# Kernel tuning notes

Hardware: AMD Instinct MI355X
Metric: run time of the kernel (lower is better)

## Reference

```python
import jax, jax.numpy as jnp
import numpy as np

M1 = M2 = M3 = 12   # Fourier modes kept per dim
WID = 32            # channel width
NL = 4              # number of Fourier layers
HID = 128           # skip-block hidden
INF = 9             # coord_dim + param_dim


def _gelu(x):
    return jax.nn.gelu(x, approximate=False)  # torch F.gelu default is exact erf


def _spectral_conv3d(x, w1, w2, w3, w4):
    # x: [B, Cin, S, V, T]; weights: [Cin, Cout, M1, M2, M3, 2]
    B, Ci, S, Vd, T = x.shape
    x_ft = jnp.fft.rfftn(x, axes=(-3, -2, -1))  # [B,Ci,S,V,T//2+1] complex64

    def cmul(sub, w):
        wc = w[..., 0] + 1j * w[..., 1]
        return jnp.einsum('bixyz,ioxyz->boxyz', sub, wc)

    Co = w1.shape[1]
    out_ft = jnp.zeros((B, Co, S, Vd, T // 2 + 1), dtype=x_ft.dtype)
    out_ft = out_ft.at[:, :, :M1, :M2, :M3].set(cmul(x_ft[:, :, :M1, :M2, :M3], w1))
    out_ft = out_ft.at[:, :, -M1:, :M2, :M3].set(cmul(x_ft[:, :, -M1:, :M2, :M3], w2))
    out_ft = out_ft.at[:, :, :M1, -M2:, :M3].set(cmul(x_ft[:, :, :M1, -M2:, :M3], w3))
    out_ft = out_ft.at[:, :, -M1:, -M2:, :M3].set(cmul(x_ft[:, :, -M1:, -M2:, :M3], w4))
    return jnp.fft.irfftn(out_ft, s=(S, Vd, T), axes=(-3, -2, -1))


def setup_inputs() -> dict:
    key = jax.random.key(0)
    ks = jax.random.split(key, 24)
    B, S, Vd, T = 4, 64, 64, 64
    scale = 1.0 / (WID * WID)
    spec_shape = (NL, WID, WID, M1, M2, M3, 2)
    inp = {
        'coords': jax.random.uniform(ks[0], (B, S, Vd, T, 3), dtype=jnp.float32),
        'params': jax.random.normal(ks[1], (B, 6), dtype=jnp.float32),
        'lift_w': 0.3 * jax.random.normal(ks[2], (INF, WID), dtype=jnp.float32),
        'lift_b': jnp.zeros((WID,), jnp.float32),
        'spec_w1': scale * jax.random.uniform(ks[3], spec_shape, dtype=jnp.float32),
        'spec_w2': scale * jax.random.uniform(ks[4], spec_shape, dtype=jnp.float32),
        'spec_w3': scale * jax.random.uniform(ks[5], spec_shape, dtype=jnp.float32),
        'spec_w4': scale * jax.random.uniform(ks[6], spec_shape, dtype=jnp.float32),
        'conv_w': 0.15 * jax.random.normal(ks[7], (NL, WID, WID), dtype=jnp.float32),
        'conv_b': jnp.zeros((NL, WID), jnp.float32),
        's1w': 0.3 * jax.random.normal(ks[8], (NL, INF, HID), dtype=jnp.float32),
        's1b': jnp.zeros((NL, HID), jnp.float32),
        's2w': 0.09 * jax.random.normal(ks[9], (NL, HID, HID), dtype=jnp.float32),
        's2b': jnp.zeros((NL, HID), jnp.float32),
        's3w': 0.09 * jax.random.normal(ks[10], (NL, HID, WID), dtype=jnp.float32),
        's3b': jnp.zeros((NL, WID), jnp.float32),
        'p1w': 0.15 * jax.random.normal(ks[11], (WID, WID // 2), dtype=jnp.float32),
        'p1b': jnp.zeros((WID // 2,), jnp.float32),
        'p2w': 0.25 * jax.random.normal(ks[12], (WID // 2, 1), dtype=jnp.float32),
        'p2b': jnp.zeros((1,), jnp.float32),
    }
    return inp


def reference(coords, params, lift_w, lift_b, spec_w1, spec_w2, spec_w3, spec_w4,
              conv_w, conv_b, s1w, s1b, s2w, s2b, s3w, s3b, p1w, p1b, p2w, p2b):
    B, S, Vd, T, _ = coords.shape
    # coordinate lift: broadcast params over grid, concat -> [B,S,V,T,9]
    pexp = jnp.broadcast_to(params[:, None, None, None, :], (B, S, Vd, T, params.shape[-1]))
    z = jnp.concatenate([coords, pexp], axis=-1)
    x = z @ lift_w + lift_b                      # [B,S,V,T,W]
    x = jnp.transpose(x, (0, 4, 1, 2, 3))        # [B,W,S,V,T]
    for i in range(NL):
        x1 = _spectral_conv3d(x, spec_w1[i], spec_w2[i], spec_w3[i], spec_w4[i])
        x2 = jnp.einsum('bixyz,oi->boxyz', x, conv_w[i]) + conv_b[i][None, :, None, None, None]
        xf = _gelu(x1 + x2)
        skip = _gelu(z @ s1w[i] + s1b[i])
        skip = _gelu(skip @ s2w[i] + s2b[i])
        skip = skip @ s3w[i] + s3b[i]            # [B,S,V,T,W]
        x = xf + jnp.transpose(skip, (0, 4, 1, 2, 3))
    x = jnp.transpose(x, (0, 2, 3, 4, 1))        # [B,S,V,T,W]
    h = _gelu(x @ p1w + p1b)
    out = (h @ p2w + p2b)[..., 0]                # [B,S,V,T]
    return out
```

## Files before the change

### kernel.cpp

```cpp
#include <hip/hip_runtime.h>
#include <hip/hip_bf16.h>
#include <math.h>

#define NB   4
#define NC   32
#define SVT  262144
#define VT   4096
#define NLAY 4
#define TWOPI_64 0.09817477042468103f

typedef __attribute__((ext_vector_type(8))) short bf16x8;
typedef __attribute__((ext_vector_type(4))) float f32x4;
typedef __attribute__((ext_vector_type(4))) unsigned short us4;

__device__ __forceinline__ float gelu_f(float x){
    float x2 = x * x;
    float u  = x * __builtin_fmaf(-0.10294322f, x2, -2.30220795f);
    float e  = __builtin_amdgcn_exp2f(u);
    return x * __builtin_amdgcn_rcpf(1.0f + e);
}

__device__ __forceinline__ unsigned short f2bf(float f){
    union { __hip_bfloat16 h; unsigned short u; } cv;
    cv.h = __float2bfloat16(f);
    return cv.u;
}
__device__ __forceinline__ float bf2f(unsigned short u){
    return __uint_as_float(((unsigned int)u) << 16);
}

__global__ __launch_bounds__(256) void k_prep(
    const float* __restrict__ params,
    const float* __restrict__ s1w, const float* __restrict__ s1b,
    const float* __restrict__ s2w, const float* __restrict__ s3w,
    unsigned short* __restrict__ w2bf,
    unsigned short* __restrict__ w3bf,
    unsigned short* __restrict__ tdft,
    unsigned short* __restrict__ T1h, unsigned short* __restrict__ T1l,
    unsigned short* __restrict__ T2h, unsigned short* __restrict__ T2l,
    float* __restrict__ pbq,
    unsigned short* __restrict__ w1dup)
{
    int g = blockIdx.x * 256 + threadIdx.x;
    if (g < 65536){
        int l = g >> 14, r = g & 16383;
        int c = r >> 7, k = r & 127;
        w2bf[g] = f2bf(s2w[l*16384 + k*128 + c]);
        return;
    }
    g -= 65536;
    if (g < 16384){
        int l = g >> 12, r = g & 4095;
        int c2 = r >> 7, k = r & 127;
        w3bf[g] = f2bf(s3w[l*4096 + k*32 + c2]);
        return;
    }
    g -= 16384;
    if (g < 2048){
        int o = g >> 6, t = g & 63;
        float val = 0.f;
        if (o < 24){
            int kz = o >> 1;
            float ang = (float)((kz * t) & 63) * TWOPI_64;
            float sn, cs; sincosf(ang, &sn, &cs);
            val = (o & 1) ? -sn : cs;
        }
        unsigned short h = f2bf(val);
        tdft[g]        = h;
        tdft[2048 + g] = f2bf(val - bf2f(h));
        return;
    }
    g -= 2048;
    if (g < 8192){
        int col = g >> 6, k1 = g & 63;
        int v = col >> 1, pout = col & 1;
        float val = 0.f;
        if (k1 < 48){
            int ky = k1 >> 1, pin = k1 & 1;
            int kya = (ky < 12) ? ky : ky + 40;
            float ang = (float)((kya * v) & 63) * TWOPI_64;
            float sn, cs; sincosf(ang, &sn, &cs);
            val = pout == 0 ? (pin == 0 ? cs : -sn) : (pin == 0 ? sn : cs);
        }
        unsigned short h = f2bf(val);
        T1h[g] = h;
        T1l[g] = f2bf(val - bf2f(h));
        return;
    }
    g -= 8192;
    if (g < 2048){
        int t = g >> 5, k2 = g & 31;
        float val = 0.f;
        if (k2 < 24){
            int kz = k2 >> 1, part = k2 & 1;
            float wk = (kz == 0) ? 1.f : 2.f;
            float ang = (float)((kz * t) & 63) * TWOPI_64;
            float sn, cs; sincosf(ang, &sn, &cs);
            val = (part ? -sn : cs) * wk * (1.f / 262144.f);
        }
        unsigned short h = f2bf(val);
        T2h[g] = h;
        T2l[g] = f2bf(val - bf2f(h));
        return;
    }
    g -= 2048;
    if (g < 2048){
        int l = g >> 9, b = (g >> 7) & 3, h = g & 127;
        float acc = s1b[l*128 + h];
        #pragma unroll
        for (int j = 0; j < 6; ++j)
            acc += params[b*6 + j] * bf2f(f2bf(s1w[l*1152 + (3 + j)*128 + h]));
        pbq[g] = acc;
        return;
    }
    g -= 2048;
    if (g < 4096){
        int l = g >> 10, rem = g & 1023;
        int h = rem >> 3, slot = rem & 7;
        float val = 0.f;
        if (slot != 3 && slot != 7){
            int row = (slot < 3) ? slot : slot - 4;
            val = bf2f(f2bf(s1w[l*1152 + row*128 + h]));
        }
        w1dup[g] = f2bf(val);
    }
}

__global__ __launch_bounds__(256) void k_lift(
    const float* __restrict__ coords, const float* __restrict__ params,
    const float* __restrict__ lw, const float* __restrict__ lb,
    float* __restrict__ x)
{
    size_t g = (size_t)blockIdx.x * 256 + threadIdx.x;
    int b = (int)(g >> 18);
    size_t p = g & (size_t)(SVT - 1);
    float z[9];
    z[0] = coords[g*3+0]; z[1] = coords[g*3+1]; z[2] = coords[g*3+2];
    #pragma unroll
    for (int j = 0; j < 6; ++j) z[3+j] = params[b*6+j];
    #pragma unroll
    for (int c = 0; c < 32; ++c){
        float acc = lb[c];
        #pragma unroll
        for (int j = 0; j < 9; ++j) acc += z[j] * lw[j*32 + c];
        x[(size_t)(b*32 + c) * SVT + p] = acc;
    }
}

__global__ __launch_bounds__(256) void k_fwdTV(
    const float* __restrict__ x, const unsigned short* __restrict__ tdft,
    float2* __restrict__ X2)
{
    __shared__ __align__(16) unsigned short Ahi[64][72], Alo[64][72];
    __shared__ __align__(16) unsigned short Bhi[32][72], Blo[32][72];
    __shared__ float2 a2[12][66];
    __shared__ float2 wtab[64];
    int tid = threadIdx.x;
    int bc = blockIdx.x >> 6;
    int s  = blockIdx.x & 63;
    if (tid < 64){
        float sn, cs;
        sincosf((float)tid * TWOPI_64, &sn, &cs);
        wtab[tid] = make_float2(cs, sn);
    }
    for (int i = tid; i < 2048; i += 256){
        int o = i >> 6, t = i & 63;
        Bhi[o][t] = tdft[i];
        Blo[o][t] = tdft[2048 + i];
    }
    {
        int row = tid >> 2, c0 = (tid & 3) << 4;
        const float* src = x + (size_t)bc * SVT + (size_t)s * VT + row*64 + c0;
        #pragma unroll
        for (int q = 0; q < 4; ++q){
            float4 v4 = *(const float4*)&src[q*4];
            float vv[4] = {v4.x, v4.y, v4.z, v4.w};
            #pragma unroll
            for (int e = 0; e < 4; ++e){
                unsigned short h = f2bf(vv[e]);
                Ahi[row][c0 + q*4 + e] = h;
                Alo[row][c0 + q*4 + e] = f2bf(vv[e] - bf2f(h));
            }
        }
    }
    __syncthreads();
    int l = tid & 63, w = tid >> 6;
    int lr = l & 15, kg = l >> 4;
    int r0 = w << 4;
    f32x4 acc[2];
    acc[0] = (f32x4){0.f,0.f,0.f,0.f}; acc[1] = (f32x4){0.f,0.f,0.f,0.f};
    #pragma unroll
    for (int kc = 0; kc < 2; ++kc){
        int ko = kc*32 + kg*8;
        bf16x8 ah = *(const bf16x8*)&Ahi[r0 + lr][ko];
        bf16x8 al = *(const bf16x8*)&Alo[r0 + lr][ko];
        #pragma unroll
        for (int n = 0; n < 2; ++n){
            bf16x8 bh = *(const bf16x8*)&Bhi[n*16 + lr][ko];
            bf16x8 bl = *(const bf16x8*)&Blo[n*16 + lr][ko];
            acc[n] = __builtin_amdgcn_mfma_f32_16x16x32_bf16(ah, bh, acc[n], 0, 0, 0);
            acc[n] = __builtin_amdgcn_mfma_f32_16x16x32_bf16(ah, bl, acc[n], 0, 0, 0);
            acc[n] = __builtin_amdgcn_mfma_f32_16x16x32_bf16(al, bh, acc[n], 0, 0, 0);
        }
    }
    #pragma unroll
    for (int n = 0; n < 2; ++n){
        int o = n*16 + lr;
        if (o < 24){
            int kz = o >> 1;
            #pragma unroll
            for (int r = 0; r < 4; ++r){
                int v = r0 + kg*4 + r;
                if (o & 1) a2[kz][v].y = acc[n][r];
                else       a2[kz][v].x = acc[n][r];
            }
        }
    }
    __syncthreads();
    for (int task = tid; task < 288; task += 256){
        int kz = task % 12;
        int ky = task / 12;
        int kya = (ky < 12) ? ky : ky + 40;
        float re = 0.f, im = 0.f;
        for (int v = 0; v < 64; ++v){
            float2 wv = wtab[(kya * v) & 63];
            float2 a  = a2[kz][v];
            re += a.x * wv.x + a.y * wv.y;
            im += a.y * wv.x - a.x * wv.y;
        }
        X2[((size_t)(bc*12 + kz) * 24 + ky) * 64 + s] = make_float2(re, im);
    }
}

__global__ __launch_bounds__(256) void k_fwdS(
    const float2* __restrict__ X2, float2* __restrict__ X3)
{
    __shared__ float2 cin[32][65];
    __shared__ float2 wtab[64];
    int tid = threadIdx.x;
    if (tid < 64){
        float sn, cs; sincosf((float)tid * TWOPI_64, &sn, &cs);
        wtab[tid] = make_float2(cs, sn);
    }
    int rbase = blockIdx.x * 32;
    for (int i = tid; i < 2048; i += 256){
        int row = i >> 6, s = i & 63;
        cin[row][s] = X2[(size_t)(rbase + row) * 64 + s];
    }
    __syncthreads();
    int row = tid & 31;
    int r = rbase + row;
    int kxg = tid >> 5;
    int kxs[3];
    #pragma unroll
    for (int j = 0; j < 3; ++j){ int kxi = kxg*3 + j; kxs[j] = (kxi < 12) ? kxi : kxi + 40; }
    float re[3] = {0,0,0}, im[3] = {0,0,0};
    for (int s = 0; s < 64; ++s){
        float2 cv = cin[row][s];
        #pragma unroll
        for (int j = 0; j < 3; ++j){
            float2 wv = wtab[(kxs[j] * s) & 63];
            re[j] += cv.x * wv.x + cv.y * wv.y;
            im[j] += cv.y * wv.x - cv.x * wv.y;
        }
    }
    int bc = r / 288; int kz = (r / 24) % 12; int ky = r % 24;
    #pragma unroll
    for (int j = 0; j < 3; ++j){
        int kxi = kxg*3 + j;
        X3[(size_t)bc * 6912 + (size_t)kxi * 288 + ky * 12 + kz] = make_float2(re[j], im[j]);
    }
}

__global__ __launch_bounds__(256) void k_modemix(
    const float2* __restrict__ X3,
    const float* __restrict__ w1, const float* __restrict__ w2,
    const float* __restrict__ w3, const float* __restrict__ w4,
    int layer, float2* __restrict__ Y)
{
    __shared__ float2 wlds[32][64];
    int tid = threadIdx.x;
    int m   = tid & 63;
    int b   = tid >> 6;
    int corner = blockIdx.y >> 3;
    int o0     = (blockIdx.y & 7) * 4;
    int moff0  = blockIdx.x * 64;
    const float* wsrc = (corner==0 ? w1 : corner==1 ? w2 : corner==2 ? w3 : w4)
                        + (size_t)layer * 3538944;
    int moff = moff0 + m;
    int m1  = moff / 144;
    int rem = moff - m1 * 144;
    int kx  = m1 + ((corner == 1 || corner == 3) ? 12 : 0);
    int mode_g = kx * 288 + rem + ((corner >= 2) ? 144 : 0);

    float xr[32], xi[32];
    const float2* xp = X3 + (size_t)b * 32 * 6912 + mode_g;
    #pragma unroll
    for (int i = 0; i < 32; ++i){
        float2 a = xp[(size_t)i * 6912];
        xr[i] = a.x; xi[i] = a.y;
    }
    for (int oo = 0; oo < 4; ++oo){
        int o = o0 + oo;
        __syncthreads();
        for (int j = tid; j < 2048; j += 256){
            int i = j >> 6, mm = j & 63;
            wlds[i][mm] = *(const float2*)&wsrc[((size_t)(i*32 + o) * 1728 + moff0 + mm) * 2];
        }
        __syncthreads();
        float re = 0.f, im = 0.f;
        #pragma unroll
        for (int i = 0; i < 32; ++i){
            float2 wv = wlds[i][m];
            re += xr[i]*wv.x - xi[i]*wv.y;
            im += xr[i]*wv.y + xi[i]*wv.x;
        }
        Y[(size_t)(b*32 + o) * 6912 + mode_g] = make_float2(re, im);
    }
}

__global__ __launch_bounds__(256) void k_invS(
    const float2* __restrict__ Y, float2* __restrict__ Z1)
{
    __shared__ float2 yin[24][24];
    __shared__ float2 wtab[64];
    int tid = threadIdx.x;
    if (tid < 64){
        float sn, cs; sincosf((float)tid * TWOPI_64, &sn, &cs);
        wtab[tid] = make_float2(cs, sn);
    }
    int bo = blockIdx.x / 12;
    int kz = blockIdx.x % 12;
    for (int i = tid; i < 576; i += 256){
        int kx = i / 24, ky = i % 24;
        yin[kx][ky] = Y[(size_t)bo * 6912 + (size_t)kx * 288 + ky * 12 + kz];
    }
    __syncthreads();
    int s = tid & 63;
    int kyg = tid >> 6;
    float re[6] = {0,0,0,0,0,0}, im[6] = {0,0,0,0,0,0};
    for (int kxi = 0; kxi < 24; ++kxi){
        int kxa = (kxi < 12) ? kxi : kxi + 40;
        float2 wv = wtab[(kxa * s) & 63];
        #pragma unroll
        for (int j = 0; j < 6; ++j){
            float2 a = yin[kxi][kyg*6 + j];
            re[j] += a.x * wv.x - a.y * wv.y;
            im[j] += a.x * wv.y + a.y * wv.x;
        }
    }
    #pragma unroll
    for (int j = 0; j < 6; ++j){
        int ky = kyg*6 + j;
        Z1[((size_t)(bo*12 + kz) * 64 + s) * 24 + ky] = make_float2(re[j], im[j]);
    }
}

__global__ __launch_bounds__(256) void k_conv(
    float* x, const float* __restrict__ cw,
    const float* __restrict__ cb, int layer)
{
    __shared__ float wsh[32][32];
    __shared__ float bsh[32];
    int tid = threadIdx.x;
    if (tid < 32) bsh[tid] = cb[layer*32 + tid];
    for (int i = tid; i < 1024; i += 256) wsh[i >> 5][i & 31] = cw[layer*1024 + i];
    __syncthreads();
    size_t g = (size_t)blockIdx.x * 256 + tid;
    int b = (int)(g >> 18);
    size_t p = g & (size_t)(SVT - 1);
    float acc[32];
    #pragma unroll
    for (int o = 0; o < 32; ++o) acc[o] = bsh[o];
    for (int i = 0; i < 32; ++i){
        float xv = x[(size_t)(b*32 + i) * SVT + p];
        #pragma unroll
        for (int o = 0; o < 32; ++o) acc[o] += xv * wsh[o][i];
    }
    #pragma unroll
    for (int o = 0; o < 32; ++o) x[(size_t)(b*32 + o) * SVT + p] = acc[o];
}

__global__ __launch_bounds__(256) void k_invVT(
    const float2* __restrict__ Z1,
    const unsigned short* __restrict__ T1h, const unsigned short* __restrict__ T1l,
    const unsigned short* __restrict__ T2h, const unsigned short* __restrict__ T2l,
    float* xio)
{
    __shared__ __align__(16) unsigned short A1h[16][72], A1l[16][72];
    __shared__ __align__(16) unsigned short A2h[64][40], A2l[64][40];
    int tid = threadIdx.x;
    int bo = blockIdx.x >> 6;
    int s  = blockIdx.x & 63;
    for (int i = tid; i < 384; i += 256){
        int r = i / 24, c = 48 + (i % 24);
        A1h[r][c] = 0; A1l[r][c] = 0;
    }
    for (int i = tid; i < 192; i += 256){
        int r = 12 + i / 48, c = i % 48;
        A1h[r][c] = 0; A1l[r][c] = 0;
    }
    for (int i = tid; i < 288; i += 256){
        int kz = i / 24, ky = i % 24;
        float2 a = Z1[((size_t)(bo*12 + kz) * 64 + s) * 24 + ky];
        unsigned short hx = f2bf(a.x), hy = f2bf(a.y);
        A1h[kz][2*ky  ] = hx; A1l[kz][2*ky  ] = f2bf(a.x - bf2f(hx));
        A1h[kz][2*ky+1] = hy; A1l[kz][2*ky+1] = f2bf(a.y - bf2f(hy));
    }
    __syncthreads();
    int l = tid & 63, w = tid >> 6;
    int lr = l & 15, kg = l >> 4;
    f32x4 acc1[2];
    acc1[0] = (f32x4){0.f,0.f,0.f,0.f}; acc1[1] = (f32x4){0.f,0.f,0.f,0.f};
    #pragma unroll
    for (int kc = 0; kc < 2; ++kc){
        int ko = kc*32 + kg*8;
        bf16x8 ah = *(const bf16x8*)&A1h[lr][ko];
        bf16x8 al = *(const bf16x8*)&A1l[lr][ko];
        #pragma unroll
        for (int n = 0; n < 2; ++n){
            int col = (2*w + n)*16 + lr;
            bf16x8 bh = *(const bf16x8*)&T1h[col*64 + ko];
            bf16x8 bl = *(const bf16x8*)&T1l[col*64 + ko];
            acc1[n] = __builtin_amdgcn_mfma_f32_16x16x32_bf16(ah, bh, acc1[n], 0, 0, 0);
            acc1[n] = __builtin_amdgcn_mfma_f32_16x16x32_bf16(ah, bl, acc1[n], 0, 0, 0);
            acc1[n] = __builtin_amdgcn_mfma_f32_16x16x32_bf16(al, bh, acc1[n], 0, 0, 0);
        }
    }
    #pragma unroll
    for (int n = 0; n < 2; ++n){
        int col = (2*w + n)*16 + lr;
        int v = col >> 1, part = col & 1;
        #pragma unroll
        for (int r = 0; r < 4; ++r){
            int k2 = 2*(kg*4 + r) + part;
            float val = acc1[n][r];
            unsigned short h = f2bf(val);
            A2h[v][k2] = h;
            A2l[v][k2] = f2bf(val - bf2f(h));
        }
    }
    int r0 = w << 4;
    bf16x8 ah2 = *(const bf16x8*)&A2h[r0 + lr][kg*8];
    bf16x8 al2 = *(const bf16x8*)&A2l[r0 + lr][kg*8];
    size_t base = (size_t)bo * SVT + (size_t)s * VT;
    #pragma unroll
    for (int n = 0; n < 4; ++n){
        f32x4 a2c = (f32x4){0.f,0.f,0.f,0.f};
        int colt = n*16 + lr;
        bf16x8 bh = *(const bf16x8*)&T2h[colt*32 + kg*8];
        bf16x8 bl = *(const bf16x8*)&T2l[colt*32 + kg*8];
        a2c = __builtin_amdgcn_mfma_f32_16x16x32_bf16(ah2, bh, a2c, 0, 0, 0);
        a2c = __builtin_amdgcn_mfma_f32_16x16x32_bf16(ah2, bl, a2c, 0, 0, 0);
        a2c = __builtin_amdgcn_mfma_f32_16x16x32_bf16(al2, bh, a2c, 0, 0, 0);
        #pragma unroll
        for (int r = 0; r < 4; ++r){
            int v = r0 + kg*4 + r;
            size_t idx = base + (size_t)v*64 + colt;
            xio[idx] = gelu_f(a2c[r] + xio[idx]);
        }
    }
}

template<int LAST>
__global__ __launch_bounds__(256, 8) void k_skip(
    const float* __restrict__ coords,
    const unsigned short* __restrict__ w1dup, const float* __restrict__ pbq,
    const unsigned short* __restrict__ w2bf, const float* __restrict__ s2b,
    const unsigned short* __restrict__ w3bf, const float* __restrict__ s3b,
    int layer, float* __restrict__ xio,
    const float* __restrict__ p1w, const float* __restrict__ p1b,
    const float* __restrict__ p2w, const float* __restrict__ p2b,
    float* __restrict__ out)
{
    __shared__ __align__(16) unsigned short A1[64][136];
    __shared__ __align__(16) unsigned short zst[4][16][8];

    int tid = threadIdx.x;
    size_t g0 = (size_t)blockIdx.x * 64;
    int b = (int)(g0 >> 18);
    const unsigned short* w2g = w2bf + (size_t)layer * 16384;
    const unsigned short* w3g = w3bf + (size_t)layer * 4096;
    const unsigned short* w1g = w1dup + (size_t)layer * 1024;
    const float* pbg = pbq + layer*512 + b*128;
    const float* b2g = s2b + layer*128;

    int l  = tid & 63;
    int w  = tid >> 6;
    int lr = l & 15;
    int kg = l >> 4;

    if (l < 16){
        size_t g = g0 + (size_t)w*16 + l;
        float z0 = coords[g*3+0], z1 = coords[g*3+1], z2 = coords[g*3+2];
        unsigned short h0 = f2bf(z0), h1 = f2bf(z1), h2 = f2bf(z2);
        bf16x8 pk;
        pk[0] = (short)h0; pk[1] = (short)h1; pk[2] = (short)h2; pk[3] = 0;
        pk[4] = (short)f2bf(z0 - bf2f(h0));
        pk[5] = (short)f2bf(z1 - bf2f(h1));
        pk[6] = (short)f2bf(z2 - bf2f(h2));
        pk[7] = 0;
        *(bf16x8*)&zst[w][l][0] = pk;
    }
    bf16x8 bz;
    if (kg == 0) bz = *(const bf16x8*)&zst[w][lr][0];
    else         bz = (bf16x8){0,0,0,0,0,0,0,0};

    {
        f32x4 accB[8];
        #pragma unroll
        for (int m = 0; m < 8; ++m) accB[m] = (f32x4){0.f,0.f,0.f,0.f};
        #pragma unroll
        for (int m = 0; m < 8; ++m){
            bf16x8 af = *(const bf16x8*)&w1g[(m*16 + lr)*8];
            accB[m] = __builtin_amdgcn_mfma_f32_16x16x32_bf16(af, bz, accB[m], 0, 0, 0);
        }
        #pragma unroll
        for (int m = 0; m < 8; ++m){
            int c0 = m*16 + kg*4;
            float4 bb = *(const float4*)&pbg[c0];
            us4 pk4;
            pk4[0] = f2bf(gelu_f(accB[m][0] + bb.x));
            pk4[1] = f2bf(gelu_f(accB[m][1] + bb.y));
            pk4[2] = f2bf(gelu_f(accB[m][2] + bb.z));
            pk4[3] = f2bf(gelu_f(accB[m][3] + bb.w));
            *(us4*)&A1[w*16 + lr][c0] = pk4;
        }
    }
    __syncthreads();

    f32x4 accC[2][4];
    #pragma unroll
    for (int mi = 0; mi < 2; ++mi)
        #pragma unroll
        for (int pt = 0; pt < 4; ++pt) accC[mi][pt] = (f32x4){0.f,0.f,0.f,0.f};
    #pragma unroll
    for (int kc = 0; kc < 4; ++kc){
        int ko = kc*32 + kg*8;
        bf16x8 a0 = *(const bf16x8*)&w2g[((2*w    )*16 + lr)*128 + ko];
        bf16x8 a1 = *(const bf16x8*)&w2g[((2*w + 1)*16 + lr)*128 + ko];
        #pragma unroll
        for (int pt = 0; pt < 4; ++pt){
            bf16x8 bb = *(const bf16x8*)&A1[pt*16 + lr][ko];
            accC[0][pt] = __builtin_amdgcn_mfma_f32_16x16x32_bf16(a0, bb, accC[0][pt], 0, 0, 0);
            accC[1][pt] = __builtin_amdgcn_mfma_f32_16x16x32_bf16(a1, bb, accC[1][pt], 0, 0, 0);
        }
    }
    __syncthreads();
    #pragma unroll
    for (int mi = 0; mi < 2; ++mi)
        #pragma unroll
        for (int pt = 0; pt < 4; ++pt){
            int c0 = (2*w + mi)*16 + kg*4;
            float4 bb = *(const float4*)&b2g[c0];
            us4 pk4;
            pk4[0] = f2bf(gelu_f(accC[mi][pt][0] + bb.x));
            pk4[1] = f2bf(gelu_f(accC[mi][pt][1] + bb.y));
            pk4[2] = f2bf(gelu_f(accC[mi][pt][2] + bb.z));
            pk4[3] = f2bf(gelu_f(accC[mi][pt][3] + bb.w));
            *(us4*)&A1[pt*16 + lr][c0] = pk4;
        }
    __syncthreads();

    int nD  = w & 1;
    int pt0 = (w >> 1) * 2;
    float b3v = s3b[layer*32 + nD*16 + lr];
    f32x4 c3[2];
    c3[0] = (f32x4){0.f,0.f,0.f,0.f}; c3[1] = (f32x4){0.f,0.f,0.f,0.f};
    #pragma unroll
    for (int kc = 0; kc < 4; ++kc){
        int ko = kc*32 + kg*8;
        bf16x8 bw3 = *(const bf16x8*)&w3g[(nD*16 + lr)*128 + ko];
        bf16x8 aa0 = *(const bf16x8*)&A1[(pt0    )*16 + lr][ko];
        bf16x8 aa1 = *(const bf16x8*)&A1[(pt0 + 1)*16 + lr][ko];
        c3[0] = __builtin_amdgcn_mfma_f32_16x16x32_bf16(aa0, bw3, c3[0], 0, 0, 0);
        c3[1] = __builtin_amdgcn_mfma_f32_16x16x32_bf16(aa1, bw3, c3[1], 0, 0, 0);
    }
    __syncthreads();

    float* outsT = (float*)&A1[0][0];
    {
        int c2 = nD*16 + lr;
        #pragma unroll
        for (int q = 0; q < 2; ++q){
            int p0 = (pt0 + q)*16 + kg*4;
            float4 v4;
            v4.x = c3[q][0] + b3v; v4.y = c3[q][1] + b3v;
            v4.z = c3[q][2] + b3v; v4.w = c3[q][3] + b3v;
            *(float4*)&outsT[c2*68 + p0] = v4;
        }
    }
    float* hs   = outsT + 2176;
    float* p1wS = outsT + 3264;
    float* smB  = outsT + 3776;
    if (LAST){
        for (int i = tid; i < 512; i += 256) p1wS[i] = p1w[i];
        if (tid < 16){ smB[tid] = p1b[tid]; smB[16 + tid] = p2w[tid]; }
        if (tid == 32) smB[32] = p2b[0];
    }
    __syncthreads();

    {
        int c  = tid >> 3;
        int pg = tid & 7;
        size_t prel = (g0 & (size_t)(SVT - 1)) + (size_t)pg*8;
        float* gp = xio + (((size_t)(b*32 + c)) << 18) + prel;
        float* op = &outsT[c*68 + pg*8];
        #pragma unroll
        for (int i = 0; i < 8; i += 4){
            float4 xv = *(const float4*)&gp[i];
            float4 ov = *(const float4*)&op[i];
            ov.x += xv.x; ov.y += xv.y; ov.z += xv.z; ov.w += xv.w;
            if (LAST) *(float4*)&op[i] = ov;
            else      *(float4*)&gp[i] = ov;
        }
    }
    if (LAST){
        __syncthreads();
        {
            int p  = tid & 63;
            int jq = tid >> 6;
            float h[4];
            #pragma unroll
            for (int j = 0; j < 4; ++j) h[j] = smB[jq*4 + j];
            for (int c = 0; c < 32; ++c){
                float xv = outsT[c*68 + p];
                #pragma unroll
                for (int j = 0; j < 4; ++j) h[j] += xv * p1wS[c*16 + jq*4 + j];
            }
            #pragma unroll
            for (int j = 0; j < 4; ++j) hs[p*17 + jq*4 + j] = h[j];
        }
        __syncthreads();
        if (tid < 64){
            float acc = smB[32];
            #pragma unroll
            for (int j = 0; j < 16; ++j) acc += gelu_f(hs[tid*17 + j]) * smB[16 + j];
            out[g0 + tid] = acc;
        }
    }
}

extern "C" void kernel_launch(void* const* d_in, const int* in_sizes, int n_in,
                              void* d_out, int out_size, void* d_ws, size_t ws_size,
                              hipStream_t stream)
{
    (void)in_sizes; (void)n_in; (void)out_size; (void)ws_size;
    const float* coords = (const float*)d_in[0];
    const float* params = (const float*)d_in[1];
    const float* lift_w = (const float*)d_in[2];
    const float* lift_b = (const float*)d_in[3];
    const float* sw1    = (const float*)d_in[4];
    const float* sw2    = (const float*)d_in[5];
    const float* sw3    = (const float*)d_in[6];
    const float* sw4    = (const float*)d_in[7];
    const float* conv_w = (const float*)d_in[8];
    const float* conv_b = (const float*)d_in[9];
    const float* s1w    = (const float*)d_in[10];
    const float* s1b    = (const float*)d_in[11];
    const float* s2w    = (const float*)d_in[12];
    const float* s2b    = (const float*)d_in[13];
    const float* s3w    = (const float*)d_in[14];
    const float* s3b    = (const float*)d_in[15];
    const float* p1w    = (const float*)d_in[16];
    const float* p1b    = (const float*)d_in[17];
    const float* p2w    = (const float*)d_in[18];
    const float* p2b    = (const float*)d_in[19];
    float* out = (float*)d_out;

    char* ws = (char*)d_ws;
    float*  xA = (float*)(ws);
    float2* X2 = (float2*)(ws + 134217728ull);
    float2* X3 = (float2*)(ws + 153092096ull);
    float2* Yb = (float2*)(ws + 160169984ull);
    unsigned short* w2bf  = (unsigned short*)(ws + 167247872ull);
    unsigned short* w3bf  = (unsigned short*)(ws + 167378944ull);
    unsigned short* tdft  = (unsigned short*)(ws + 167411712ull);
    unsigned short* T1h   = (unsigned short*)(ws + 167419904ull);
    unsigned short* T1l   = (unsigned short*)(ws + 167436288ull);
    unsigned short* T2h   = (unsigned short*)(ws + 167452672ull);
    unsigned short* T2l   = (unsigned short*)(ws + 167456768ull);
    float*          pbq   = (float*)(ws + 167460864ull);
    unsigned short* w1dup = (unsigned short*)(ws + 167469056ull);

    k_prep<<<392, 256, 0, stream>>>(params, s1w, s1b, s2w, s3w,
                                    w2bf, w3bf, tdft, T1h, T1l, T2h, T2l,
                                    pbq, w1dup);
    k_lift<<<4096, 256, 0, stream>>>(coords, params, lift_w, lift_b, xA);

    for (int l = 0; l < NLAY; ++l){
        k_fwdTV<<<8192, 256, 0, stream>>>(xA, tdft, X2);
        k_fwdS<<<1152, 256, 0, stream>>>(X2, X3);
        dim3 gmm(27, 32);
        k_modemix<<<gmm, 256, 0, stream>>>(X3, sw1, sw2, sw3, sw4, l, Yb);
        k_invS<<<1536, 256, 0, stream>>>(Yb, X2);
        k_conv<<<4096, 256, 0, stream>>>(xA, conv_w, conv_b, l);
        k_invVT<<<8192, 256, 0, stream>>>(X2, T1h, T1l, T2h, T2l, xA);
        if (l < NLAY - 1)
            k_skip<0><<<16384, 256, 0, stream>>>(coords, w1dup, pbq,
                w2bf, s2b, w3bf, s3b, l, xA, p1w, p1b, p2w, p2b, out);
        else
            k_skip<1><<<16384, 256, 0, stream>>>(coords, w1dup, pbq,
                w2bf, s2b, w3bf, s3b, l, xA, p1w, p1b, p2w, p2b, out);
    }
}
```

Before: 1.701 ms.

## Fuse pointwise channel conv into inverse V/T DFT kernel using MFMA

Replaces the separate 1x1 channel-mixing kernel and the inverse V/T transform kernel with a single kernel. Each block converts its slice of x into split-bf16 in LDS and does the 32x32 channel mix on MFMA with precomputed hi/lo conv weights. It also computes the inverse ky DFT with scalar FMAs, then runs the T-transform MFMA and applies bias, residual add and GELU in one pass. This removes a full read and write of the activation tensor per layer. In exchange, spectral data is re-read redundantly across blocks, the ky DFT moves from MFMA to scalar code, and the kernel updates x in place through restrict-qualified pointers.

```diff
diff --git a/kernel.cpp b/kernel.cpp
--- a/kernel.cpp
+++ b/kernel.cpp
@@ -33,13 +33,15 @@
     const float* __restrict__ params,
     const float* __restrict__ s1w, const float* __restrict__ s1b,
     const float* __restrict__ s2w, const float* __restrict__ s3w,
+    const float* __restrict__ conv_w,
     unsigned short* __restrict__ w2bf,
     unsigned short* __restrict__ w3bf,
     unsigned short* __restrict__ tdft,
     unsigned short* __restrict__ T1h, unsigned short* __restrict__ T1l,
     unsigned short* __restrict__ T2h, unsigned short* __restrict__ T2l,
     float* __restrict__ pbq,
-    unsigned short* __restrict__ w1dup)
+    unsigned short* __restrict__ w1dup,
+    unsigned short* __restrict__ wcvh, unsigned short* __restrict__ wcvl)
 {
     int g = blockIdx.x * 256 + threadIdx.x;
     if (g < 65536){
@@ -123,6 +125,14 @@
             val = bf2f(f2bf(s1w[l*1152 + row*128 + h]));
         }
         w1dup[g] = f2bf(val);
+        return;
+    }
+    g -= 4096;
+    if (g < 4096){
+        float val = conv_w[g];
+        unsigned short h = f2bf(val);
+        wcvh[g] = h;
+        wcvl[g] = f2bf(val - bf2f(h));
     }
 }
 
@@ -356,108 +366,124 @@
     }
 }
 
-__global__ __launch_bounds__(256) void k_conv(
-    float* x, const float* __restrict__ cw,
-    const float* __restrict__ cb, int layer)
-{
-    __shared__ float wsh[32][32];
-    __shared__ float bsh[32];
+__global__ __launch_bounds__(256) void k_cinvVT(
+    const float* __restrict__ xin, const float2* __restrict__ Z1,
+    const unsigned short* __restrict__ T2h, const unsigned short* __restrict__ T2l,
+    const unsigned short* __restrict__ wcvh, const unsigned short* __restrict__ wcvl,
+    const float* __restrict__ cb, int layer, float* __restrict__ xout)
+{
+    __shared__ __align__(16) unsigned short XT[2][256][40];
+    __shared__ __align__(16) unsigned short A2h[128][40], A2l[128][40];
+    __shared__ float2 wtab[64];
     int tid = threadIdx.x;
-    if (tid < 32) bsh[tid] = cb[layer*32 + tid];
-    for (int i = tid; i < 1024; i += 256) wsh[i >> 5][i & 31] = cw[layer*1024 + i];
-    __syncthreads();
-    size_t g = (size_t)blockIdx.x * 256 + tid;
-    int b = (int)(g >> 18);
-    size_t p = g & (size_t)(SVT - 1);
-    float acc[32];
-    #pragma unroll
-    for (int o = 0; o < 32; ++o) acc[o] = bsh[o];
-    for (int i = 0; i < 32; ++i){
-        float xv = x[(size_t)(b*32 + i) * SVT + p];
-        #pragma unroll
-        for (int o = 0; o < 32; ++o) acc[o] += xv * wsh[o][i];
-    }
-    #pragma unroll
-    for (int o = 0; o < 32; ++o) x[(size_t)(b*32 + o) * SVT + p] = acc[o];
-}
-
-__global__ __launch_bounds__(256) void k_invVT(
-    const float2* __restrict__ Z1,
-    const unsigned short* __restrict__ T1h, const unsigned short* __restrict__ T1l,
-    const unsigned short* __restrict__ T2h, const unsigned short* __restrict__ T2l,
-    float* xio)
-{
-    __shared__ __align__(16) unsigned short A1h[16][72], A1l[16][72];
-    __shared__ __align__(16) unsigned short A2h[64][40], A2l[64][40];
-    int tid = threadIdx.x;
-    int bo = blockIdx.x >> 6;
-    int s  = blockIdx.x & 63;
-    for (int i = tid; i < 384; i += 256){
-        int r = i / 24, c = 48 + (i % 24);
-        A1h[r][c] = 0; A1l[r][c] = 0;
-    }
-    for (int i = tid; i < 192; i += 256){
-        int r = 12 + i / 48, c = i % 48;
-        A1h[r][c] = 0; A1l[r][c] = 0;
-    }
-    for (int i = tid; i < 288; i += 256){
-        int kz = i / 24, ky = i % 24;
-        float2 a = Z1[((size_t)(bo*12 + kz) * 64 + s) * 24 + ky];
-        unsigned short hx = f2bf(a.x), hy = f2bf(a.y);
-        A1h[kz][2*ky  ] = hx; A1l[kz][2*ky  ] = f2bf(a.x - bf2f(hx));
-        A1h[kz][2*ky+1] = hy; A1l[kz][2*ky+1] = f2bf(a.y - bf2f(hy));
-    }
-    __syncthreads();
-    int l = tid & 63, w = tid >> 6;
-    int lr = l & 15, kg = l >> 4;
-    f32x4 acc1[2];
-    acc1[0] = (f32x4){0.f,0.f,0.f,0.f}; acc1[1] = (f32x4){0.f,0.f,0.f,0.f};
-    #pragma unroll
-    for (int kc = 0; kc < 2; ++kc){
-        int ko = kc*32 + kg*8;
-        bf16x8 ah = *(const bf16x8*)&A1h[lr][ko];
-        bf16x8 al = *(const bf16x8*)&A1l[lr][ko];
-        #pragma unroll
-        for (int n = 0; n < 2; ++n){
-            int col = (2*w + n)*16 + lr;
-            bf16x8 bh = *(const bf16x8*)&T1h[col*64 + ko];
-            bf16x8 bl = *(const bf16x8*)&T1l[col*64 + ko];
-            acc1[n] = __builtin_amdgcn_mfma_f32_16x16x32_bf16(ah, bh, acc1[n], 0, 0, 0);
-            acc1[n] = __builtin_amdgcn_mfma_f32_16x16x32_bf16(ah, bl, acc1[n], 0, 0, 0);
-            acc1[n] = __builtin_amdgcn_mfma_f32_16x16x32_bf16(al, bh, acc1[n], 0, 0, 0);
-        }
-    }
-    #pragma unroll
-    for (int n = 0; n < 2; ++n){
-        int col = (2*w + n)*16 + lr;
-        int v = col >> 1, part = col & 1;
-        #pragma unroll
-        for (int r = 0; r < 4; ++r){
-            int k2 = 2*(kg*4 + r) + part;
-            float val = acc1[n][r];
-            unsigned short h = f2bf(val);
-            A2h[v][k2] = h;
-            A2l[v][k2] = f2bf(val - bf2f(h));
-        }
-    }
-    int r0 = w << 4;
-    bf16x8 ah2 = *(const bf16x8*)&A2h[r0 + lr][kg*8];
-    bf16x8 al2 = *(const bf16x8*)&A2l[r0 + lr][kg*8];
-    size_t base = (size_t)bo * SVT + (size_t)s * VT;
-    #pragma unroll
-    for (int n = 0; n < 4; ++n){
-        f32x4 a2c = (f32x4){0.f,0.f,0.f,0.f};
-        int colt = n*16 + lr;
-        bf16x8 bh = *(const bf16x8*)&T2h[colt*32 + kg*8];
-        bf16x8 bl = *(const bf16x8*)&T2l[colt*32 + kg*8];
-        a2c = __builtin_amdgcn_mfma_f32_16x16x32_bf16(ah2, bh, a2c, 0, 0, 0);
-        a2c = __builtin_amdgcn_mfma_f32_16x16x32_bf16(ah2, bl, a2c, 0, 0, 0);
-        a2c = __builtin_amdgcn_mfma_f32_16x16x32_bf16(al2, bh, a2c, 0, 0, 0);
-        #pragma unroll
-        for (int r = 0; r < 4; ++r){
-            int v = r0 + kg*4 + r;
-            size_t idx = base + (size_t)v*64 + colt;
-            xio[idx] = gelu_f(a2c[r] + xio[idx]);
+    int vg = blockIdx.x & 15;
+    int s  = (blockIdx.x >> 4) & 63;
+    int b  = blockIdx.x >> 10;
+    if (tid < 64){
+        float sn, cs; sincosf((float)tid * TWOPI_64, &sn, &cs);
+        wtab[tid] = make_float2(cs, sn);
+    }
+    {
+        int row = tid >> 1, half = tid & 1;
+        us4 z = (us4){0,0,0,0};
+        *(us4*)&A2h[row][24 + half*4] = z;
+        *(us4*)&A2l[row][24 + half*4] = z;
+    }
+    {
+        const float* xp = xin + (size_t)b*32*SVT + (size_t)s*VT + (size_t)vg*256 + tid;
+        #pragma unroll
+        for (int q = 0; q < 4; ++q){
+            bf16x8 ph, pl;
+            #pragma unroll
+            for (int e = 0; e < 8; ++e){
+                float v = xp[(size_t)(q*8 + e) * SVT];
+                unsigned short h = f2bf(v);
+                ph[e] = (short)h;
+                pl[e] = (short)f2bf(v - bf2f(h));
+            }
+            *(bf16x8*)&XT[0][tid][q*8] = ph;
+            *(bf16x8*)&XT[1][tid][q*8] = pl;
+        }
+    }
+    __syncthreads();
+    #pragma unroll
+    for (int j = 0; j < 6; ++j){
+        int task = tid + j*256;
+        int o = task / 48, rem = task % 48;
+        int kz = rem >> 2, vloc = rem & 3;
+        int v = vg*4 + vloc;
+        const float2* zp = Z1 + ((size_t)((b*32 + o)*12 + kz) * 64 + s) * 24;
+        float re = 0.f, im = 0.f;
+        #pragma unroll
+        for (int ky = 0; ky < 24; ++ky){
+            int kya = (ky < 12) ? ky : ky + 40;
+            float2 wv = wtab[(kya * v) & 63];
+            float2 a = zp[ky];
+            re += a.x * wv.x - a.y * wv.y;
+            im += a.x * wv.y + a.y * wv.x;
+        }
+        int row = o*4 + vloc;
+        unsigned short hr = f2bf(re), hm = f2bf(im);
+        A2h[row][2*kz  ] = hr; A2l[row][2*kz  ] = f2bf(re - bf2f(hr));
+        A2h[row][2*kz+1] = hm; A2l[row][2*kz+1] = f2bf(im - bf2f(hm));
+    }
+    __syncthreads();
+    int l = tid & 63, w = tid >> 6, lr = l & 15, kg = l >> 4;
+    f32x4 dcv[2][4];
+    #pragma unroll
+    for (int ot = 0; ot < 2; ++ot){
+        bf16x8 ah = *(const bf16x8*)&wcvh[layer*1024 + (ot*16 + lr)*32 + kg*8];
+        bf16x8 al = *(const bf16x8*)&wcvl[layer*1024 + (ot*16 + lr)*32 + kg*8];
+        #pragma unroll
+        for (int ptt = 0; ptt < 4; ++ptt){
+            bf16x8 bh = *(const bf16x8*)&XT[0][w*64 + ptt*16 + lr][kg*8];
+            bf16x8 bl = *(const bf16x8*)&XT[1][w*64 + ptt*16 + lr][kg*8];
+            f32x4 d = (f32x4){0.f,0.f,0.f,0.f};
+            d = __builtin_amdgcn_mfma_f32_16x16x32_bf16(ah, bh, d, 0, 0, 0);
+            d = __builtin_amdgcn_mfma_f32_16x16x32_bf16(ah, bl, d, 0, 0, 0);
+            d = __builtin_amdgcn_mfma_f32_16x16x32_bf16(al, bh, d, 0, 0, 0);
+            dcv[ot][ptt] = d;
+        }
+    }
+    __syncthreads();
+    float* x2s = (float*)&XT[0][0][0];
+    #pragma unroll
+    for (int ot = 0; ot < 2; ++ot)
+        #pragma unroll
+        for (int ptt = 0; ptt < 4; ++ptt)
+            #pragma unroll
+            for (int r = 0; r < 4; ++r)
+                x2s[(ot*16 + kg*4 + r)*266 + w*64 + ptt*16 + lr] = dcv[ot][ptt][r];
+    f32x4 dt[2][4];
+    #pragma unroll
+    for (int rt = 0; rt < 2; ++rt){
+        bf16x8 ah = *(const bf16x8*)&A2h[w*32 + rt*16 + lr][kg*8];
+        bf16x8 al = *(const bf16x8*)&A2l[w*32 + rt*16 + lr][kg*8];
+        #pragma unroll
+        for (int n = 0; n < 4; ++n){
+            bf16x8 bh = *(const bf16x8*)&T2h[(n*16 + lr)*32 + kg*8];
+            bf16x8 bl = *(const bf16x8*)&T2l[(n*16 + lr)*32 + kg*8];
+            f32x4 d = (f32x4){0.f,0.f,0.f,0.f};
+            d = __builtin_amdgcn_mfma_f32_16x16x32_bf16(ah, bh, d, 0, 0, 0);
+            d = __builtin_amdgcn_mfma_f32_16x16x32_bf16(ah, bl, d, 0, 0, 0);
+            d = __builtin_amdgcn_mfma_f32_16x16x32_bf16(al, bh, d, 0, 0, 0);
+            dt[rt][n] = d;
+        }
+    }
+    __syncthreads();
+    size_t outb = (size_t)b*32*SVT + (size_t)s*VT + (size_t)vg*256;
+    #pragma unroll
+    for (int rt = 0; rt < 2; ++rt){
+        int o = 8*w + rt*4 + kg;
+        float cbv = cb[layer*32 + o];
+        #pragma unroll
+        for (int n = 0; n < 4; ++n){
+            #pragma unroll
+            for (int r = 0; r < 4; ++r){
+                int pt = r*64 + n*16 + lr;
+                float val = dt[rt][n][r] + x2s[o*266 + pt] + cbv;
+                xout[outb + (size_t)o*SVT + pt] = gelu_f(val);
+            }
         }
     }
 }
@@ -682,10 +708,12 @@
     unsigned short* T2l   = (unsigned short*)(ws + 167456768ull);
     float*          pbq   = (float*)(ws + 167460864ull);
     unsigned short* w1dup = (unsigned short*)(ws + 167469056ull);
-
-    k_prep<<<392, 256, 0, stream>>>(params, s1w, s1b, s2w, s3w,
+    unsigned short* wcvh  = (unsigned short*)(ws + 167477248ull);
+    unsigned short* wcvl  = (unsigned short*)(ws + 167485440ull);
+
+    k_prep<<<408, 256, 0, stream>>>(params, s1w, s1b, s2w, s3w, conv_w,
                                     w2bf, w3bf, tdft, T1h, T1l, T2h, T2l,
-                                    pbq, w1dup);
+                                    pbq, w1dup, wcvh, wcvl);
     k_lift<<<4096, 256, 0, stream>>>(coords, params, lift_w, lift_b, xA);
 
     for (int l = 0; l < NLAY; ++l){
@@ -694,8 +722,8 @@
         dim3 gmm(27, 32);
         k_modemix<<<gmm, 256, 0, stream>>>(X3, sw1, sw2, sw3, sw4, l, Yb);
         k_invS<<<1536, 256, 0, stream>>>(Yb, X2);
-        k_conv<<<4096, 256, 0, stream>>>(xA, conv_w, conv_b, l);
-        k_invVT<<<8192, 256, 0, stream>>>(X2, T1h, T1l, T2h, T2l, xA);
+        k_cinvVT<<<4096, 256, 0, stream>>>(xA, X2, T2h, T2l, wcvh, wcvl,
+                                           conv_b, l, xA);
         if (l < NLAY - 1)
             k_skip<0><<<16384, 256, 0, stream>>>(coords, w1dup, pbq,
                 w2bf, s2b, w3bf, s3b, l, xA, p1w, p1b, p2w, p2b, out);
```

Result: faster. 1.582 ms (-7.0%).
